# Performance work log

Measured on AMD Instinct MI355X. Metric: run time of the kernel, lower is better.

Reference implementation:

```python
import jax, jax.numpy as jnp
import numpy as np

D_MODEL = 512
N_HEADS = 16
D_HEAD = D_MODEL // N_HEADS


def _relative_shift(pos_score):
    # pos_score: [B, H, T, T]  (Transformer-XL shift trick)
    B, H, T1, T2 = pos_score.shape
    padded = jnp.pad(pos_score, ((0, 0), (0, 0), (0, 0), (1, 0)))  # [B,H,T1,T2+1]
    padded = padded.reshape(B, H, T2 + 1, T1)
    return padded[:, :, 1:].reshape(B, H, T1, T2)


def setup_inputs() -> dict:
    key = jax.random.key(0)
    ks = jax.random.split(key, 12)
    B, T, D = 4, 1024, D_MODEL
    s = 1.0 / np.sqrt(D)
    return {
        "q": jax.random.normal(ks[0], (B, T, D), jnp.float32),
        "k": jax.random.normal(ks[1], (B, T, D), jnp.float32),
        "v": jax.random.normal(ks[2], (B, T, D), jnp.float32),
        "pos_embedding": jax.random.normal(ks[3], (B, T, D), jnp.float32),
        "Wq": jax.random.normal(ks[4], (D, D), jnp.float32) * s,
        "bq": jnp.zeros((D,), jnp.float32),
        "Wp": jax.random.normal(ks[5], (D, D), jnp.float32) * s,
        "Wf": jax.random.normal(ks[6], (D, D), jnp.float32) * s,
        "bf": jnp.zeros((D,), jnp.float32),
        "u_bias": jax.random.normal(ks[7], (N_HEADS, D_HEAD), jnp.float32) * s,
        "v_bias": jax.random.normal(ks[8], (N_HEADS, D_HEAD), jnp.float32) * s,
    }


def reference(q, k, v, pos_embedding, Wq, bq, Wp, Wf, bf, u_bias, v_bias):
    B, T, D = q.shape
    H, Dh = N_HEADS, D_HEAD
    sqrt_dim = jnp.asarray(np.sqrt(D_MODEL), q.dtype)
    # NOTE: original module uses linear_q for q, k AND v (faithful to source)
    qh = (q @ Wq + bq).reshape(B, T, H, Dh)            # [B,T,H,Dh]
    kh = (k @ Wq + bq).reshape(B, T, H, Dh)
    vh = (v @ Wq + bq).reshape(B, T, H, Dh)
    ph = (pos_embedding @ Wp).reshape(B, T, H, Dh)     # no bias

    content_score = jnp.einsum('bthd,bshd->bhts', qh + u_bias, kh)
    pos_score = jnp.einsum('bthd,bshd->bhts', qh + v_bias, ph)
    pos_score = _relative_shift(pos_score)

    score = (content_score + pos_score) / sqrt_dim     # [B,H,T,T]
    attn = jax.nn.softmax(score, axis=-1)              # dropout identity in eval
    context = jnp.einsum('bhts,bshd->bthd', attn, vh).reshape(B, T, D)
    return context @ Wf + bf
```

## Files before the change

### kernel.cpp

```cpp
#include <hip/hip_runtime.h>
#include <hip/hip_bf16.h>

typedef __bf16 bf16;
typedef bf16 bf16x8 __attribute__((ext_vector_type(8)));
typedef bf16 bf16x4 __attribute__((ext_vector_type(4)));
typedef float f32x4 __attribute__((ext_vector_type(4)));
typedef _Float16 f16x4 __attribute__((ext_vector_type(4)));

#define SCALE_LOG2 0.06376237f


__global__ __launch_bounds__(256) void prep_kernel(
    const float* __restrict__ Wq, const float* __restrict__ Wp, const float* __restrict__ Wf,
    bf16* __restrict__ WqT, bf16* __restrict__ WpT, bf16* __restrict__ WfT)
{
  const int tid = threadIdx.x;
  __shared__ bf16 t[64][72];
  const int m = blockIdx.x >> 6;
  const int tb = blockIdx.x & 63;
  const int tr = tb >> 3, tc = tb & 7;
  const float* W = (m == 0) ? Wq : (m == 1) ? Wp : Wf;
  bf16*        O = (m == 0) ? WqT : (m == 1) ? WpT : WfT;
  const int r = tid >> 2, cg = tid & 3;
  {
    const float* src = W + (size_t)(tr * 64 + r) * 512 + tc * 64 + cg * 16;
    f32x4 a = *(const f32x4*)src, b2 = *(const f32x4*)(src + 4);
    f32x4 c = *(const f32x4*)(src + 8), d = *(const f32x4*)(src + 12);
    bf16x8 lo, hi;
#pragma unroll
    for (int j = 0; j < 4; j++) { lo[j] = (bf16)a[j]; lo[4 + j] = (bf16)b2[j]; hi[j] = (bf16)c[j]; hi[4 + j] = (bf16)d[j]; }
    *(bf16x8*)(&t[r][cg * 16])     = lo;
    *(bf16x8*)(&t[r][cg * 16 + 8]) = hi;
  }
  __syncthreads();
  bf16x8 o0, o1;
#pragma unroll
  for (int j = 0; j < 8; j++) { o0[j] = t[cg * 16 + j][r]; o1[j] = t[cg * 16 + 8 + j][r]; }
  bf16* dst = O + (size_t)(tc * 64 + r) * 512 + tr * 64 + cg * 16;
  *(bf16x8*)dst = o0;
  *(bf16x8*)(dst + 8) = o1;
}

__global__ __launch_bounds__(256) void proj_gemm(
    const float* __restrict__ q, const float* __restrict__ k, const float* __restrict__ v,
    const float* __restrict__ pos,
    const bf16* __restrict__ WqT, const bf16* __restrict__ WpT, const float* __restrict__ bq,
    bf16* __restrict__ qh, bf16* __restrict__ kh, bf16* __restrict__ vT, bf16* __restrict__ phx)
{
  __shared__ bf16 ABs[2 * 128 * 72];
  bf16* As = ABs;
  bf16* Bs = ABs + 128 * 72;
  bf16* vtile = ABs;
  const int tid = threadIdx.x;
  const int wave = tid >> 6, lane = tid & 63, quad = lane >> 4, ln = lane & 15;
  const int wg = blockIdx.x;
  const int xcd = wg & 7, sidx = wg >> 3;
  const int tn = sidx & 3;
  const int tm = xcd + ((sidx >> 2) << 3);
  const int kind = tm >> 5;
  const int rr0 = (tm & 31) * 128;
  const float* X = (kind == 0) ? q : (kind == 1) ? k : (kind == 2) ? v : pos;
  const bf16* WT = ((kind < 3) ? WqT : WpT) + (size_t)tn * 128 * 512;
  const int qn_ = (wave & 1) * 64;
  const int qr_ = (wave >> 1) * 64;
  const int srow = tid >> 2, scg = tid & 3;

  f32x4 acc[4][4] = {};

  f32x4  xa0[4], xa1[4];
  bf16x8 wr0[2], wr1[2];
  {
    const float* p0 = X + (size_t)(rr0 + srow) * 512 + scg * 16;
    const float* p1 = X + (size_t)(rr0 + srow + 64) * 512 + scg * 16;
#pragma unroll
    for (int u = 0; u < 4; u++) { xa0[u] = *(const f32x4*)(p0 + u * 4); xa1[u] = *(const f32x4*)(p1 + u * 4); }
    const bf16* w0 = WT + (size_t)srow * 512 + scg * 16;
    const bf16* w1 = WT + (size_t)(srow + 64) * 512 + scg * 16;
    wr0[0] = *(const bf16x8*)w0; wr0[1] = *(const bf16x8*)(w0 + 8);
    wr1[0] = *(const bf16x8*)w1; wr1[1] = *(const bf16x8*)(w1 + 8);
  }

  for (int kk = 0; kk < 8; kk++) {
    __syncthreads();
    {
      bf16x8 lo, hi;
#pragma unroll
      for (int j = 0; j < 4; j++) { lo[j] = (bf16)xa0[0][j]; lo[4 + j] = (bf16)xa0[1][j]; hi[j] = (bf16)xa0[2][j]; hi[4 + j] = (bf16)xa0[3][j]; }
      *(bf16x8*)(As + srow * 72 + scg * 16)     = lo;
      *(bf16x8*)(As + srow * 72 + scg * 16 + 8) = hi;
#pragma unroll
      for (int j = 0; j < 4; j++) { lo[j] = (bf16)xa1[0][j]; lo[4 + j] = (bf16)xa1[1][j]; hi[j] = (bf16)xa1[2][j]; hi[4 + j] = (bf16)xa1[3][j]; }
      *(bf16x8*)(As + (srow + 64) * 72 + scg * 16)     = lo;
      *(bf16x8*)(As + (srow + 64) * 72 + scg * 16 + 8) = hi;
      *(bf16x8*)(Bs + srow * 72 + scg * 16)            = wr0[0];
      *(bf16x8*)(Bs + srow * 72 + scg * 16 + 8)        = wr0[1];
      *(bf16x8*)(Bs + (srow + 64) * 72 + scg * 16)     = wr1[0];
      *(bf16x8*)(Bs + (srow + 64) * 72 + scg * 16 + 8) = wr1[1];
    }
    __syncthreads();

    if (kk < 7) {
      const int k0n = (kk + 1) * 64;
      const float* p0 = X + (size_t)(rr0 + srow) * 512 + k0n + scg * 16;
      const float* p1 = X + (size_t)(rr0 + srow + 64) * 512 + k0n + scg * 16;
#pragma unroll
      for (int u = 0; u < 4; u++) { xa0[u] = *(const f32x4*)(p0 + u * 4); xa1[u] = *(const f32x4*)(p1 + u * 4); }
      const bf16* w0 = WT + (size_t)srow * 512 + k0n + scg * 16;
      const bf16* w1 = WT + (size_t)(srow + 64) * 512 + k0n + scg * 16;
      wr0[0] = *(const bf16x8*)w0; wr0[1] = *(const bf16x8*)(w0 + 8);
      wr1[0] = *(const bf16x8*)w1; wr1[1] = *(const bf16x8*)(w1 + 8);
    }

#pragma unroll
    for (int ks = 0; ks < 2; ks++) {
      bf16x8 wf[4], xf[4];
#pragma unroll
      for (int i = 0; i < 4; i++) {
        wf[i] = *(const bf16x8*)(Bs + (qn_ + i * 16 + ln) * 72 + ks * 32 + quad * 8);
        xf[i] = *(const bf16x8*)(As + (qr_ + i * 16 + ln) * 72 + ks * 32 + quad * 8);
      }
#pragma unroll
      for (int i = 0; i < 4; i++)
#pragma unroll
        for (int j = 0; j < 4; j++)
          acc[i][j] = __builtin_amdgcn_mfma_f32_16x16x32_bf16(wf[i], xf[j], acc[i][j], 0, 0, 0);
    }
  }
  __syncthreads();

  if (kind == 2) {
#pragma unroll
    for (int i = 0; i < 4; i++) {
      const int nloc = qn_ + i * 16 + quad * 4;
      f32x4 b4 = *(const f32x4*)(bq + tn * 128 + nloc);
#pragma unroll
      for (int j = 0; j < 4; j++) {
        const int mloc = qr_ + j * 16 + ln;
        bf16x4 pk;
#pragma unroll
        for (int r = 0; r < 4; r++) pk[r] = (bf16)(acc[i][j][r] + b4[r]);
        *(bf16x4*)(vtile + mloc * 132 + nloc) = pk;
      }
    }
    __syncthreads();
    const int n = tid >> 1, mh = (tid & 1) * 64;
    const int bb2 = rr0 >> 10, tt0 = rr0 & 1023;
    bf16* vdst = vT + ((size_t)(bb2 * 16 + tn * 4 + (n >> 5)) * 32 + (n & 31)) * 1024 + tt0 + mh;
#pragma unroll
    for (int c = 0; c < 8; c++) {
      bf16x8 oc;
#pragma unroll
      for (int e = 0; e < 8; e++) oc[e] = vtile[(mh + c * 8 + e) * 132 + n];
      *(bf16x8*)(vdst + c * 8) = oc;
    }
  } else {
#pragma unroll
    for (int i = 0; i < 4; i++) {
      const int nn0 = tn * 128 + qn_ + i * 16 + quad * 4;
      const int dd0 = nn0 & 31, hh = nn0 >> 5;
      f32x4 b4 = {0.f, 0.f, 0.f, 0.f};
      if (kind < 3) b4 = *(const f32x4*)(bq + nn0);
#pragma unroll
      for (int j = 0; j < 4; j++) {
        const int rr = rr0 + qr_ + j * 16 + ln;
        const int bb = rr >> 10, tt = rr & 1023;
        const size_t base = (size_t)(bb * 16 + hh);
        bf16x4 pk;
#pragma unroll
        for (int r = 0; r < 4; r++) pk[r] = (bf16)(acc[i][j][r] + b4[r]);
        if (kind == 0)      *(bf16x4*)(qh + (base * 1024 + tt) * 32 + dd0) = pk;
        else if (kind == 1) *(bf16x4*)(kh + (base * 1024 + tt) * 32 + dd0) = pk;
        else {
          *(bf16x4*)(phx + (base * 2048 + tt) * 32 + dd0) = pk;
          if (tt <= 1021) *(bf16x4*)(phx + (base * 2048 + tt + 1025) * 32 + dd0) = pk;
          if (tt == 1023) {
            bf16x4 zz = {};
            *(bf16x4*)(phx + (base * 2048 + 1024) * 32 + dd0) = zz;
            *(bf16x4*)(phx + (base * 2048 + 2047) * 32 + dd0) = zz;
          }
        }
      }
    }
  }
}

__global__ __launch_bounds__(256, 4) void attn_kernel(
    const bf16* __restrict__ qh, const bf16* __restrict__ kh,
    const bf16* __restrict__ vT, const bf16* __restrict__ phx,
    const float* __restrict__ u_bias, const float* __restrict__ v_bias,
    bf16* __restrict__ ctx)
{
  __shared__ bf16     kst[64 * 40];
  __shared__ bf16     phs[128 * 40];
  __shared__ bf16     vst[32 * 72];
  __shared__ _Float16 fs[4 * 16 * 84];
  __shared__ bf16     pb[4 * 16 * 72];

  const int tid = threadIdx.x;
  const int wave = tid >> 6, lane = tid & 63, quad = lane >> 4, ln = lane & 15;
  const int wg = blockIdx.x;
  const int bh = wg & 63;
  const int tq = wg >> 6;
  const int h = bh & 15, b = bh >> 4;
  const int t0 = tq * 64;
  const bf16* qh_h  = qh  + (size_t)bh * 1024 * 32;
  const bf16* kh_h  = kh  + (size_t)bh * 1024 * 32;
  const bf16* vT_h  = vT  + (size_t)bh * 32 * 1024;
  const bf16* phx_h = phx + (size_t)bh * 2048 * 32;

  _Float16* fsw = fs + wave * 16 * 84;
  bf16*     pbw = pb + wave * 16 * 72;

  const int sr4 = tid >> 2, sc4 = tid & 3;
  const int sr8 = tid >> 3, sc8 = tid & 7;

  const int Ab  = quad * 4 + ((15 - ln) & ~3);
  const int msh = ((15 - ln) & 3) * 16;

  bf16x8 qu, qva, qvn;
  {
    const int t = t0 + wave * 16 + ln;
    bf16x8 q0 = *(const bf16x8*)(qh_h + (size_t)t * 32 + quad * 8);
    bf16x8 q1 = *(const bf16x8*)(qh_h + (size_t)(t + 1) * 32 + quad * 8);
    const float* ubp = u_bias + h * 32 + quad * 8;
    const float* vbp = v_bias + h * 32 + quad * 8;
#pragma unroll
    for (int j = 0; j < 8; j++) {
      qu[j]  = (bf16)(((float)q0[j] + ubp[j]) * SCALE_LOG2);
      qva[j] = (bf16)(((float)q0[j] + vbp[j]) * SCALE_LOG2);
      qvn[j] = (bf16)(((float)q1[j] + vbp[j]) * SCALE_LOG2);
    }
  }

  f32x4 O0 = {0.f, 0.f, 0.f, 0.f}, O1 = {0.f, 0.f, 0.f, 0.f};
  float l_lane = 0.0f;
  const f32x4 zf = {0.f, 0.f, 0.f, 0.f};

  bf16x8 g0, g1, g2, g3;
  {
    const int jbp = -t0 + 960;
    g0 = *(const bf16x8*)(kh_h  + (size_t)sr4 * 32 + sc4 * 8);
    g1 = *(const bf16x8*)(phx_h + (size_t)(jbp + sr4) * 32 + sc4 * 8);
    g2 = *(const bf16x8*)(phx_h + (size_t)(jbp + 64 + sr4) * 32 + sc4 * 8);
    g3 = *(const bf16x8*)(vT_h  + (size_t)sr8 * 1024 + sc8 * 8);
  }

  for (int si = 0; si < 16; si++) {
    const int s0 = si * 64;
    const int jbase = s0 - t0 + 960;
    const int jb0 = jbase + (3 - wave) * 16;

    __syncthreads();

    *(bf16x8*)(kst + sr4 * 40 + sc4 * 8)        = g0;
    *(bf16x8*)(phs + sr4 * 40 + sc4 * 8)        = g1;
    *(bf16x8*)(phs + (64 + sr4) * 40 + sc4 * 8) = g2;
    *(bf16x8*)(vst + sr8 * 72 + sc8 * 8)        = g3;

    __syncthreads();

    if (si != 15) {
      const int s0n = s0 + 64, jbn = jbase + 64;
      g0 = *(const bf16x8*)(kh_h  + (size_t)(s0n + sr4) * 32 + sc4 * 8);
      g1 = *(const bf16x8*)(phx_h + (size_t)(jbn + sr4) * 32 + sc4 * 8);
      g2 = *(const bf16x8*)(phx_h + (size_t)(jbn + 64 + sr4) * 32 + sc4 * 8);
      g3 = *(const bf16x8*)(vT_h  + (size_t)sr8 * 1024 + s0n + sc8 * 8);
    }

#pragma unroll
    for (int i = 0; i < 5; i++) {
      const int row = (3 - wave + i) * 16 + ln;
      bf16x8 pbf = *(const bf16x8*)(phs + row * 40 + quad * 8);
      bf16x8 bsel = (jb0 + i * 16 >= 1024) ? qvn : qva;
      f32x4 f = __builtin_amdgcn_mfma_f32_16x16x32_bf16(pbf, bsel, zf, 0, 0, 0);
      f16x4 fh;
#pragma unroll
      for (int r = 0; r < 4; r++) fh[r] = (_Float16)f[r];
      *(f16x4*)(fsw + ln * 84 + i * 16 + quad * 4) = fh;
    }

    f32x4 c[4];
#pragma unroll
    for (int cs = 0; cs < 4; cs++) {
      bf16x8 kbf = *(const bf16x8*)(kst + (cs * 16 + ln) * 40 + quad * 8);
      c[cs] = __builtin_amdgcn_mfma_f32_16x16x32_bf16(kbf, qu, zf, 0, 0, 0);
    }

    const _Float16* rowp = fsw + ln * 84;
#pragma unroll
    for (int cs = 0; cs < 4; cs++) {
      const uint64_t v0 = *(const uint64_t*)(rowp + cs * 16 + Ab);
      const uint64_t v1 = *(const uint64_t*)(rowp + cs * 16 + Ab + 4);
      union { uint64_t u; f16x4 v; } W;
      W.u = (v0 >> msh) | ((v1 << 1) << (63 - msh));
      bf16x4 pk;
#pragma unroll
      for (int r = 0; r < 4; r++) {
        const float p = __builtin_amdgcn_exp2f(c[cs][r] + (float)W.v[r]);
        l_lane += p;
        pk[r] = (bf16)p;
      }
      *(bf16x4*)(pbw + ln * 72 + cs * 16 + quad * 4) = pk;
    }

#pragma unroll
    for (int kb = 0; kb < 2; kb++) {
      bf16x8 a  = *(const bf16x8*)(pbw + ln * 72 + kb * 32 + quad * 8);
      bf16x8 b0 = *(const bf16x8*)(vst + ln * 72 + kb * 32 + quad * 8);
      bf16x8 b1 = *(const bf16x8*)(vst + (16 + ln) * 72 + kb * 32 + quad * 8);
      O0 = __builtin_amdgcn_mfma_f32_16x16x32_bf16(a, b0, O0, 0, 0, 0);
      O1 = __builtin_amdgcn_mfma_f32_16x16x32_bf16(a, b1, O1, 0, 0, 0);
    }
  }

  l_lane += __shfl_xor(l_lane, 16);
  l_lane += __shfl_xor(l_lane, 32);
#pragma unroll
  for (int r = 0; r < 4; r++) {
    const float lr = __shfl(l_lane, quad * 4 + r);
    const float inv = 1.0f / lr;
    const int t = t0 + wave * 16 + quad * 4 + r;
    const size_t o = ((size_t)(b * 1024 + t)) * 512 + h * 32;
    ctx[o + ln]      = (bf16)(O0[r] * inv);
    ctx[o + 16 + ln] = (bf16)(O1[r] * inv);
  }
}

__global__ __launch_bounds__(256) void out_gemm(
    const bf16* __restrict__ ctx, const bf16* __restrict__ WfT,
    const float* __restrict__ bfv, float* __restrict__ out)
{
  __shared__ bf16 As[32 * 40];
  __shared__ bf16 Bs[128 * 40];
  const int tid = threadIdx.x;
  const int wave = tid >> 6, lane = tid & 63, quad = lane >> 4, ln = lane & 15;
  const int wg = blockIdx.x;
  const int xcd = wg & 7, sidx = wg >> 3;
  const int tn = sidx & 3;
  const int tm = xcd + ((sidx >> 2) << 3);
  const int rr0 = tm * 32;
  const bf16* WT = WfT + (size_t)tn * 128 * 512;
  const int qm = (wave & 1) * 16, qn = (wave >> 1) * 64;
  const int srow = tid >> 2, scg = tid & 3;
  const int srow8 = tid >> 3, scg8 = tid & 7;

  bf16x4 a4;
  bf16x8 b0r, b1r;
  {
    a4  = *(const bf16x4*)(ctx + (size_t)(rr0 + srow8) * 512 + scg8 * 4);
    b0r = *(const bf16x8*)(WT + (size_t)srow * 512 + scg * 8);
    b1r = *(const bf16x8*)(WT + (size_t)(srow + 64) * 512 + scg * 8);
  }

  f32x4 acc[4] = {};
  for (int kk = 0; kk < 16; kk++) {
    __syncthreads();
    *(bf16x4*)(As + srow8 * 40 + scg8 * 4)      = a4;
    *(bf16x8*)(Bs + srow * 40 + scg * 8)        = b0r;
    *(bf16x8*)(Bs + (srow + 64) * 40 + scg * 8) = b1r;
    __syncthreads();

    if (kk < 15) {
      const int k0n = (kk + 1) * 32;
      a4  = *(const bf16x4*)(ctx + (size_t)(rr0 + srow8) * 512 + k0n + scg8 * 4);
      b0r = *(const bf16x8*)(WT + (size_t)srow * 512 + k0n + scg * 8);
      b1r = *(const bf16x8*)(WT + (size_t)(srow + 64) * 512 + k0n + scg * 8);
    }

    bf16x8 af, bfm[4];
    af = *(const bf16x8*)(As + (qm + ln) * 40 + quad * 8);
#pragma unroll
    for (int j = 0; j < 4; j++)
      bfm[j] = *(const bf16x8*)(Bs + (qn + j * 16 + ln) * 40 + quad * 8);
#pragma unroll
    for (int j = 0; j < 4; j++)
      acc[j] = __builtin_amdgcn_mfma_f32_16x16x32_bf16(af, bfm[j], acc[j], 0, 0, 0);
  }

#pragma unroll
  for (int j = 0; j < 4; j++) {
    const int nn = tn * 128 + qn + j * 16 + ln;
    const float bias = bfv[nn];
#pragma unroll
    for (int r = 0; r < 4; r++) {
      const int rr = rr0 + qm + quad * 4 + r;
      out[(size_t)rr * 512 + nn] = acc[j][r] + bias;
    }
  }
}

extern "C" void kernel_launch(void* const* d_in, const int* in_sizes, int n_in,
                              void* d_out, int out_size, void* d_ws, size_t ws_size,
                              hipStream_t stream) {
  const float* q   = (const float*)d_in[0];
  const float* k   = (const float*)d_in[1];
  const float* v   = (const float*)d_in[2];
  const float* pe  = (const float*)d_in[3];
  const float* Wq  = (const float*)d_in[4];
  const float* bq  = (const float*)d_in[5];
  const float* Wp  = (const float*)d_in[6];
  const float* Wf  = (const float*)d_in[7];
  const float* bfv = (const float*)d_in[8];
  const float* ub  = (const float*)d_in[9];
  const float* vb  = (const float*)d_in[10];

  bf16* ws  = (bf16*)d_ws;
  bf16* qh  = ws;
  bf16* kh  = qh + 2097152;
  bf16* vT  = kh + 2097152;
  bf16* phx = vT + 2097152;
  bf16* WqT = phx + 4194304;
  bf16* WpT = WqT + 262144;
  bf16* WfT = WpT + 262144;
  bf16* ctx = WfT + 262144;

  prep_kernel<<<192, 256, 0, stream>>>(Wq, Wp, Wf, WqT, WpT, WfT);
  proj_gemm<<<512, 256, 0, stream>>>(q, k, v, pe, WqT, WpT, bq, qh, kh, vT, phx);
  attn_kernel<<<1024, 256, 0, stream>>>(qh, kh, vT, phx, ub, vb, ctx);
  out_gemm<<<512, 256, 0, stream>>>(ctx, WfT, bfv, (float*)d_out);
}
```

Measured before the change: 158.9 us.

## Load K and pos tiles directly from global, double-buffer V in LDS

K and shifted positional tiles are no longer staged through shared memory; each wave reads its MFMA operands straight from global (L1/L2-cached) memory. V is double-buffered in LDS so only one barrier per iteration is needed instead of two. This removes LDS store traffic and one sync per tile. In exchange the K and pos loads now sit on the critical path with global latency and no register prefetch, and several waves re-read overlapping pos rows from cache.

Result: no change. 157.9 us (-0.6%).

```diff
diff --git a/kernel.cpp b/kernel.cpp
--- a/kernel.cpp
+++ b/kernel.cpp
@@ -190,9 +190,7 @@
     const float* __restrict__ u_bias, const float* __restrict__ v_bias,
     bf16* __restrict__ ctx)
 {
-  __shared__ bf16     kst[64 * 40];
-  __shared__ bf16     phs[128 * 40];
-  __shared__ bf16     vst[32 * 72];
+  __shared__ bf16     vst[2][32 * 72];
   __shared__ _Float16 fs[4 * 16 * 84];
   __shared__ bf16     pb[4 * 16 * 72];
 
@@ -211,7 +209,6 @@
   _Float16* fsw = fs + wave * 16 * 84;
   bf16*     pbw = pb + wave * 16 * 72;
 
-  const int sr4 = tid >> 2, sc4 = tid & 3;
   const int sr8 = tid >> 3, sc8 = tid & 7;
 
   const int Ab  = quad * 4 + ((15 - ln) & ~3);
@@ -236,41 +233,24 @@
   float l_lane = 0.0f;
   const f32x4 zf = {0.f, 0.f, 0.f, 0.f};
 
-  bf16x8 g0, g1, g2, g3;
-  {
-    const int jbp = -t0 + 960;
-    g0 = *(const bf16x8*)(kh_h  + (size_t)sr4 * 32 + sc4 * 8);
-    g1 = *(const bf16x8*)(phx_h + (size_t)(jbp + sr4) * 32 + sc4 * 8);
-    g2 = *(const bf16x8*)(phx_h + (size_t)(jbp + 64 + sr4) * 32 + sc4 * 8);
-    g3 = *(const bf16x8*)(vT_h  + (size_t)sr8 * 1024 + sc8 * 8);
-  }
+  bf16x8 g3 = *(const bf16x8*)(vT_h + (size_t)sr8 * 1024 + sc8 * 8);
 
   for (int si = 0; si < 16; si++) {
     const int s0 = si * 64;
     const int jbase = s0 - t0 + 960;
     const int jb0 = jbase + (3 - wave) * 16;
-
-    __syncthreads();
-
-    *(bf16x8*)(kst + sr4 * 40 + sc4 * 8)        = g0;
-    *(bf16x8*)(phs + sr4 * 40 + sc4 * 8)        = g1;
-    *(bf16x8*)(phs + (64 + sr4) * 40 + sc4 * 8) = g2;
-    *(bf16x8*)(vst + sr8 * 72 + sc8 * 8)        = g3;
-
-    __syncthreads();
-
-    if (si != 15) {
-      const int s0n = s0 + 64, jbn = jbase + 64;
-      g0 = *(const bf16x8*)(kh_h  + (size_t)(s0n + sr4) * 32 + sc4 * 8);
-      g1 = *(const bf16x8*)(phx_h + (size_t)(jbn + sr4) * 32 + sc4 * 8);
-      g2 = *(const bf16x8*)(phx_h + (size_t)(jbn + 64 + sr4) * 32 + sc4 * 8);
-      g3 = *(const bf16x8*)(vT_h  + (size_t)sr8 * 1024 + s0n + sc8 * 8);
-    }
+    bf16* vc = vst[si & 1];
+
+    *(bf16x8*)(vc + sr8 * 72 + sc8 * 8) = g3;
+
+    __syncthreads();
+
+    if (si != 15)
+      g3 = *(const bf16x8*)(vT_h + (size_t)sr8 * 1024 + s0 + 64 + sc8 * 8);
 
 #pragma unroll
     for (int i = 0; i < 5; i++) {
-      const int row = (3 - wave + i) * 16 + ln;
-      bf16x8 pbf = *(const bf16x8*)(phs + row * 40 + quad * 8);
+      bf16x8 pbf = *(const bf16x8*)(phx_h + (size_t)(jb0 + i * 16 + ln) * 32 + quad * 8);
       bf16x8 bsel = (jb0 + i * 16 >= 1024) ? qvn : qva;
       f32x4 f = __builtin_amdgcn_mfma_f32_16x16x32_bf16(pbf, bsel, zf, 0, 0, 0);
       f16x4 fh;
@@ -282,7 +262,7 @@
     f32x4 c[4];
 #pragma unroll
     for (int cs = 0; cs < 4; cs++) {
-      bf16x8 kbf = *(const bf16x8*)(kst + (cs * 16 + ln) * 40 + quad * 8);
+      bf16x8 kbf = *(const bf16x8*)(kh_h + (size_t)(s0 + cs * 16 + ln) * 32 + quad * 8);
       c[cs] = __builtin_amdgcn_mfma_f32_16x16x32_bf16(kbf, qu, zf, 0, 0, 0);
     }
 
@@ -306,8 +286,8 @@
 #pragma unroll
     for (int kb = 0; kb < 2; kb++) {
       bf16x8 a  = *(const bf16x8*)(pbw + ln * 72 + kb * 32 + quad * 8);
-      bf16x8 b0 = *(const bf16x8*)(vst + ln * 72 + kb * 32 + quad * 8);
-      bf16x8 b1 = *(const bf16x8*)(vst + (16 + ln) * 72 + kb * 32 + quad * 8);
+      bf16x8 b0 = *(const bf16x8*)(vc + ln * 72 + kb * 32 + quad * 8);
+      bf16x8 b1 = *(const bf16x8*)(vc + (16 + ln) * 72 + kb * 32 + quad * 8);
       O0 = __builtin_amdgcn_mfma_f32_16x16x32_bf16(a, b0, O0, 0, 0, 0);
       O1 = __builtin_amdgcn_mfma_f32_16x16x32_bf16(a, b1, O1, 0, 0, 0);
     }
```
